# Kernel optimization log

Measured on AMD Instinct MI355X. Metric: run time of the kernel, lower is better.

The kernel has to match this reference:

```python
import jax, jax.numpy as jnp
import numpy as np

D_MODEL = 1024
D_FF = 4 * D_MODEL
NUM_EXPERTS = 8
TOP_K = 2
B, L = 4, 2048


def setup_inputs() -> dict:
    key = jax.random.key(0)
    ks = jax.random.split(key, 7)
    s = 0.02
    return {
        "x": jax.random.normal(ks[0], (B, L, D_MODEL), dtype=jnp.float32),
        "Wr": jax.random.normal(ks[1], (D_MODEL, NUM_EXPERTS), dtype=jnp.float32) * s,
        "br": jnp.zeros((NUM_EXPERTS,), dtype=jnp.float32),
        "W1": jax.random.normal(ks[2], (NUM_EXPERTS, D_MODEL, D_FF), dtype=jnp.float32) * s,
        "b1": jnp.zeros((NUM_EXPERTS, D_FF), dtype=jnp.float32),
        "W2": jax.random.normal(ks[3], (NUM_EXPERTS, D_FF, D_MODEL), dtype=jnp.float32) * s,
        "b2": jnp.zeros((NUM_EXPERTS, D_MODEL), dtype=jnp.float32),
    }


def reference(x, Wr, br, W1, b1, W2, b2):
    Bb, Ll, D = x.shape
    x_flat = x.reshape(-1, D)                      # [T, D]
    T = x_flat.shape[0]

    # Router: softmax over experts, then top-k and renormalize (matches torch)
    logits = x_flat @ Wr + br                      # [T, E]
    probs = jax.nn.softmax(logits, axis=-1)
    topk_w, topk_idx = jax.lax.top_k(probs, TOP_K)  # [T, K]
    topk_w = topk_w / jnp.sum(topk_w, axis=-1, keepdims=True)

    # Per-token per-expert combine weights: w_full[t, e] = sum_k topk_w[t,k] * (topk_idx[t,k]==e)
    # (top_k indices are distinct, so scatter-add equals the masked-overwrite loop)
    w_full = jnp.zeros((T, NUM_EXPERTS), dtype=x.dtype)
    rows = jnp.arange(T)[:, None]
    w_full = w_full.at[rows, topk_idx].add(topk_w)

    # Dense all-expert MLP (same math as masked per-expert dispatch; dropout is eval/no-op)
    h = jax.nn.gelu(jnp.einsum("td,edf->etf", x_flat, W1) + b1[:, None, :], approximate=False)
    y = jnp.einsum("etf,efd->etd", h, W2) + b2[:, None, :]   # [E, T, D]
    out = jnp.einsum("te,etd->td", w_full, y)                # [T, D]
    return out.reshape(Bb, Ll, D)
```

## Files before the change

### kernel.cpp

```cpp
#include <hip/hip_runtime.h>
#include <hip/hip_bf16.h>

#define T_TOKENS 8192
#define DM 1024
#define DF 4096
#define NE 8
#define NROWS 16384

typedef __attribute__((ext_vector_type(8))) short bf16x8;
typedef __attribute__((ext_vector_type(4))) float f32x4;

__device__ inline unsigned short f2bf(float f) {
  unsigned int u = __builtin_bit_cast(unsigned int, f);
  u = (u + 0x7fffu + ((u >> 16) & 1u)) >> 16;
  return (unsigned short)u;
}

__device__ inline float bf2f(unsigned short s) {
  unsigned int u = ((unsigned int)s) << 16;
  return __builtin_bit_cast(float, u);
}

__device__ __forceinline__ void gload16(const unsigned short* g, unsigned short* l) {
  __builtin_amdgcn_global_load_lds(
      (const __attribute__((address_space(1))) unsigned int*)g,
      (__attribute__((address_space(3))) unsigned int*)l,
      16, 0, 0);
}

__global__ void router_kernel(const float* __restrict__ x,
                              const float* __restrict__ Wr,
                              const float* __restrict__ br,
                              int* __restrict__ ctrl,
                              int* __restrict__ tope,
                              float* __restrict__ topw,
                              unsigned short* __restrict__ xb) {
  const int wid = threadIdx.x >> 6;
  const int lane = threadIdx.x & 63;
  const int t = blockIdx.x * 4 + wid;
  const float* xr = x + (size_t)t * DM;
  unsigned short* xbr = xb + (size_t)t * DM;
  float a[NE];
#pragma unroll
  for (int e = 0; e < NE; ++e) a[e] = 0.f;
#pragma unroll
  for (int it = 0; it < 4; ++it) {
    const int d0 = it * 256 + lane * 4;
    const float4 xv = *(const float4*)(xr + d0);
    ushort4 o;
    o.x = f2bf(xv.x); o.y = f2bf(xv.y); o.z = f2bf(xv.z); o.w = f2bf(xv.w);
    *(ushort4*)(xbr + d0) = o;
    const float xs[4] = {xv.x, xv.y, xv.z, xv.w};
#pragma unroll
    for (int j = 0; j < 4; ++j) {
      const float4 wa = *(const float4*)(Wr + (size_t)(d0 + j) * NE);
      const float4 wb = *(const float4*)(Wr + (size_t)(d0 + j) * NE + 4);
      a[0] += xs[j] * wa.x; a[1] += xs[j] * wa.y;
      a[2] += xs[j] * wa.z; a[3] += xs[j] * wa.w;
      a[4] += xs[j] * wb.x; a[5] += xs[j] * wb.y;
      a[6] += xs[j] * wb.z; a[7] += xs[j] * wb.w;
    }
  }
#pragma unroll
  for (int off = 32; off > 0; off >>= 1) {
#pragma unroll
    for (int e = 0; e < NE; ++e) a[e] += __shfl_xor(a[e], off);
  }
  if (lane == 0) {
    float lg[NE];
    float m = -1e30f;
#pragma unroll
    for (int e = 0; e < NE; ++e) { lg[e] = a[e] + br[e]; m = fmaxf(m, lg[e]); }
    float p[NE];
#pragma unroll
    for (int e = 0; e < NE; ++e) p[e] = expf(lg[e] - m);
    int i0 = 0;
#pragma unroll
    for (int e = 1; e < NE; ++e) if (p[e] > p[i0]) i0 = e;
    int i1 = (i0 == 0) ? 1 : 0;
#pragma unroll
    for (int e = 0; e < NE; ++e) if (e != i0 && p[e] > p[i1]) i1 = e;
    const float s = p[i0] + p[i1];
    tope[2 * t] = i0;
    tope[2 * t + 1] = i1;
    topw[2 * t] = p[i0] / s;
    topw[2 * t + 1] = p[i1] / s;
    atomicAdd(&ctrl[i0], 1);
    atomicAdd(&ctrl[i1], 1);
  }
}

__global__ void scan_kernel(int* __restrict__ ctrl) {
  if (threadIdx.x == 0 && blockIdx.x == 0) {
    int off = 0;
    for (int e = 0; e < NE; ++e) {
      ctrl[8 + e] = off;
      ctrl[20 + e] = off;
      off += ctrl[e];
    }
    ctrl[16] = off;
  }
}

__global__ void place_kernel(const int* __restrict__ tope,
                             const float* __restrict__ topw,
                             int* __restrict__ ctrl,
                             int* __restrict__ rowlist,
                             float* __restrict__ roww,
                             int* __restrict__ posmap) {
  const int t = blockIdx.x * blockDim.x + threadIdx.x;
#pragma unroll
  for (int k = 0; k < 2; ++k) {
    const int e = tope[2 * t + k];
    const int pos = atomicAdd(&ctrl[20 + e], 1);
    rowlist[pos] = t;
    roww[pos] = topw[2 * t + k];
    posmap[2 * t + k] = pos;
  }
}

__global__ void transpose_cvt_kernel(const float* __restrict__ in,
                                     unsigned short* __restrict__ outp,
                                     int R, int C) {
  __shared__ float tile[64][65];
  const int e = blockIdx.z;
  const int r0 = blockIdx.y * 64;
  const int c0 = blockIdx.x * 64;
  const float* src = in + ((size_t)e * R + r0) * C + c0;
#pragma unroll
  for (int i = 0; i < 16; ++i) {
    const int rr = (threadIdx.x >> 6) + i * 4;
    const int cc = threadIdx.x & 63;
    tile[rr][cc] = src[(size_t)rr * C + cc];
  }
  __syncthreads();
  unsigned short* dst = outp + ((size_t)e * C + c0) * R + r0;
#pragma unroll
  for (int i = 0; i < 8; ++i) {
    const int rr = (threadIdx.x >> 5) + i * 8;
    const int cc = (threadIdx.x & 31) * 2;
    const unsigned int lo = f2bf(tile[cc][rr]);
    const unsigned int hi = f2bf(tile[cc + 1][rr]);
    *(unsigned int*)(dst + (size_t)rr * R + cc) = lo | (hi << 16);
  }
}

__global__ __launch_bounds__(256, 2) void gemm1_kernel(
    const unsigned short* __restrict__ xb,
    const unsigned short* __restrict__ w1t,
    const float* __restrict__ b1,
    const int* __restrict__ ctrl,
    const int* __restrict__ rowlist,
    unsigned short* __restrict__ h) {
  const int e = blockIdx.z;
  const int count = ctrl[e];
  const int mt = blockIdx.y;
  if (mt * 128 >= count) return;
  const int off = ctrl[8 + e];
  const int n0 = blockIdx.x * 128;
  const int tid = threadIdx.x;
  const int wid = tid >> 6;
  const int lane = tid & 63;
  const int wm = (wid & 1) * 64;
  const int wn = (wid >> 1) * 64;
  const int q = lane >> 4;
  const int l16 = lane & 15;
  const int rl = lane >> 3;
  const int ch = lane & 7;

  __shared__ __attribute__((aligned(16))) unsigned short lA[128 * 64];
  __shared__ __attribute__((aligned(16))) unsigned short lB[128 * 64];

  const unsigned short* aBase[4];
  const unsigned short* bBase[4];
  unsigned short* lABase[4];
  unsigned short* lBBase[4];
#pragma unroll
  for (int i = 0; i < 4; ++i) {
    const int r = wid * 32 + i * 8 + rl;
    int rr = mt * 128 + r;
    if (rr >= count) rr = count - 1;
    const int tok = rowlist[off + rr];
    aBase[i] = xb + (size_t)tok * DM + ch * 8;
    bBase[i] = w1t + ((size_t)e * DF + n0 + r) * DM + ch * 8;
    lABase[i] = &lA[(wid * 32 + i * 8) * 64];
    lBBase[i] = &lB[(wid * 32 + i * 8) * 64];
  }

  f32x4 acc[4][4];
  const f32x4 z = {0.f, 0.f, 0.f, 0.f};
#pragma unroll
  for (int im = 0; im < 4; ++im)
#pragma unroll
    for (int in = 0; in < 4; ++in) acc[im][in] = z;

  for (int k0 = 0; k0 < DM; k0 += 64) {
#pragma unroll
    for (int i = 0; i < 4; ++i) gload16(aBase[i] + k0, lABase[i]);
#pragma unroll
    for (int i = 0; i < 4; ++i) gload16(bBase[i] + k0, lBBase[i]);
    __syncthreads();
#pragma unroll
    for (int ks = 0; ks < 2; ++ks) {
      bf16x8 af[4], bfr[4];
#pragma unroll
      for (int im = 0; im < 4; ++im)
        af[im] = *(const bf16x8*)&lA[(wm + im * 16 + l16) * 64 + ks * 32 + q * 8];
#pragma unroll
      for (int in = 0; in < 4; ++in)
        bfr[in] = *(const bf16x8*)&lB[(wn + in * 16 + l16) * 64 + ks * 32 + q * 8];
#pragma unroll
      for (int im = 0; im < 4; ++im)
#pragma unroll
        for (int in = 0; in < 4; ++in)
          acc[im][in] = __builtin_amdgcn_mfma_f32_16x16x32_bf16(
              af[im], bfr[in], acc[im][in], 0, 0, 0);
    }
    __syncthreads();
  }

#pragma unroll
  for (int in = 0; in < 4; ++in) {
    const int col = n0 + wn + in * 16 + l16;
    const float bias = b1[(size_t)e * DF + col];
#pragma unroll
    for (int im = 0; im < 4; ++im) {
      const int rbase = mt * 128 + wm + im * 16 + q * 4;
#pragma unroll
      for (int r2 = 0; r2 < 4; ++r2) {
        const int r = rbase + r2;
        if (r < count) {
          const float v = acc[im][in][r2] + bias;
          const float g = 0.5f * v * (1.0f + erff(v * 0.70710678118f));
          h[((size_t)(off + r)) * DF + col] = f2bf(g);
        }
      }
    }
  }
}

__global__ __launch_bounds__(256, 2) void gemm2_kernel(
    const unsigned short* __restrict__ h,
    const unsigned short* __restrict__ w2t,
    const float* __restrict__ b2,
    const int* __restrict__ ctrl,
    unsigned short* __restrict__ y) {
  const int e = blockIdx.z;
  const int count = ctrl[e];
  const int mt = blockIdx.y;
  if (mt * 128 >= count) return;
  const int off = ctrl[8 + e];
  const int n0 = blockIdx.x * 128;
  const int tid = threadIdx.x;
  const int wid = tid >> 6;
  const int lane = tid & 63;
  const int wm = (wid & 1) * 64;
  const int wn = (wid >> 1) * 64;
  const int q = lane >> 4;
  const int l16 = lane & 15;
  const int rl = lane >> 3;
  const int ch = lane & 7;

  __shared__ __attribute__((aligned(16))) unsigned short lA[128 * 64];
  __shared__ __attribute__((aligned(16))) unsigned short lB[128 * 64];

  const unsigned short* aBase[4];
  const unsigned short* bBase[4];
  unsigned short* lABase[4];
  unsigned short* lBBase[4];
#pragma unroll
  for (int i = 0; i < 4; ++i) {
    const int r = wid * 32 + i * 8 + rl;
    int rr = mt * 128 + r;
    if (rr >= count) rr = count - 1;
    aBase[i] = h + (size_t)(off + rr) * DF + ch * 8;
    bBase[i] = w2t + ((size_t)e * DM + n0 + r) * DF + ch * 8;
    lABase[i] = &lA[(wid * 32 + i * 8) * 64];
    lBBase[i] = &lB[(wid * 32 + i * 8) * 64];
  }

  f32x4 acc[4][4];
  const f32x4 z = {0.f, 0.f, 0.f, 0.f};
#pragma unroll
  for (int im = 0; im < 4; ++im)
#pragma unroll
    for (int in = 0; in < 4; ++in) acc[im][in] = z;

  for (int k0 = 0; k0 < DF; k0 += 64) {
#pragma unroll
    for (int i = 0; i < 4; ++i) gload16(aBase[i] + k0, lABase[i]);
#pragma unroll
    for (int i = 0; i < 4; ++i) gload16(bBase[i] + k0, lBBase[i]);
    __syncthreads();
#pragma unroll
    for (int ks = 0; ks < 2; ++ks) {
      bf16x8 af[4], bfr[4];
#pragma unroll
      for (int im = 0; im < 4; ++im)
        af[im] = *(const bf16x8*)&lA[(wm + im * 16 + l16) * 64 + ks * 32 + q * 8];
#pragma unroll
      for (int in = 0; in < 4; ++in)
        bfr[in] = *(const bf16x8*)&lB[(wn + in * 16 + l16) * 64 + ks * 32 + q * 8];
#pragma unroll
      for (int im = 0; im < 4; ++im)
#pragma unroll
        for (int in = 0; in < 4; ++in)
          acc[im][in] = __builtin_amdgcn_mfma_f32_16x16x32_bf16(
              af[im], bfr[in], acc[im][in], 0, 0, 0);
    }
    __syncthreads();
  }

#pragma unroll
  for (int in = 0; in < 4; ++in) {
    const int col = n0 + wn + in * 16 + l16;
    const float bias = b2[(size_t)e * DM + col];
#pragma unroll
    for (int im = 0; im < 4; ++im) {
      const int rbase = mt * 128 + wm + im * 16 + q * 4;
#pragma unroll
      for (int r2 = 0; r2 < 4; ++r2) {
        const int r = rbase + r2;
        if (r < count) {
          y[(size_t)(off + r) * DM + col] = f2bf(acc[im][in][r2] + bias);
        }
      }
    }
  }
}

__global__ void combine_kernel(const unsigned short* __restrict__ y,
                               const int* __restrict__ posmap,
                               const float* __restrict__ topw,
                               float* __restrict__ out) {
  const int t = blockIdx.x;
  const int c = threadIdx.x * 4;
  const int p0 = posmap[2 * t];
  const int p1 = posmap[2 * t + 1];
  const float w0 = topw[2 * t];
  const float w1 = topw[2 * t + 1];
  const ushort4 a = *(const ushort4*)(y + (size_t)p0 * DM + c);
  const ushort4 b = *(const ushort4*)(y + (size_t)p1 * DM + c);
  float4 o;
  o.x = w0 * bf2f(a.x) + w1 * bf2f(b.x);
  o.y = w0 * bf2f(a.y) + w1 * bf2f(b.y);
  o.z = w0 * bf2f(a.z) + w1 * bf2f(b.z);
  o.w = w0 * bf2f(a.w) + w1 * bf2f(b.w);
  *(float4*)(out + (size_t)t * DM + c) = o;
}

extern "C" void kernel_launch(void* const* d_in, const int* in_sizes, int n_in,
                              void* d_out, int out_size, void* d_ws, size_t ws_size,
                              hipStream_t stream) {
  const float* x  = (const float*)d_in[0];
  const float* Wr = (const float*)d_in[1];
  const float* br = (const float*)d_in[2];
  const float* W1 = (const float*)d_in[3];
  const float* b1 = (const float*)d_in[4];
  const float* W2 = (const float*)d_in[5];
  const float* b2 = (const float*)d_in[6];
  float* out = (float*)d_out;

  char* p = (char*)d_ws;
  auto alloc = [&](size_t bytes) -> char* {
    char* r = p;
    p += (bytes + 255) & ~(size_t)255;
    return r;
  };
  int* ctrl = (int*)alloc(1024);
  int* tope = (int*)alloc((size_t)2 * T_TOKENS * 4);
  float* topw = (float*)alloc((size_t)2 * T_TOKENS * 4);
  int* rowlist = (int*)alloc((size_t)NROWS * 4);
  float* roww = (float*)alloc((size_t)NROWS * 4);
  int* posmap = (int*)alloc((size_t)NROWS * 4);
  unsigned short* xb  = (unsigned short*)alloc((size_t)T_TOKENS * DM * 2);
  unsigned short* w1t = (unsigned short*)alloc((size_t)NE * DF * DM * 2);
  unsigned short* w2t = (unsigned short*)alloc((size_t)NE * DM * DF * 2);
  unsigned short* h   = (unsigned short*)alloc((size_t)NROWS * DF * 2);
  if ((size_t)(p - (char*)d_ws) > ws_size) return;

  unsigned short* y = w1t;

  hipMemsetAsync(ctrl, 0, 1024, stream);

  router_kernel<<<T_TOKENS / 4, 256, 0, stream>>>(x, Wr, br, ctrl, tope, topw, xb);
  scan_kernel<<<1, 64, 0, stream>>>(ctrl);
  place_kernel<<<T_TOKENS / 256, 256, 0, stream>>>(tope, topw, ctrl, rowlist, roww, posmap);
  transpose_cvt_kernel<<<dim3(DF / 64, DM / 64, NE), 256, 0, stream>>>(W1, w1t, DM, DF);
  transpose_cvt_kernel<<<dim3(DM / 64, DF / 64, NE), 256, 0, stream>>>(W2, w2t, DF, DM);
  gemm1_kernel<<<dim3(DF / 128, 64, NE), 256, 0, stream>>>(xb, w1t, b1, ctrl, rowlist, h);
  gemm2_kernel<<<dim3(DM / 128, 64, NE), 256, 0, stream>>>(h, w2t, b2, ctrl, y);
  combine_kernel<<<T_TOKENS, 256, 0, stream>>>(y, posmap, topw, out);
}
```

Before: 1.122 ms.

## Swizzle LDS tiles, transpose MFMA operands for vector stores, raise occupancy

Applies an XOR swizzle to the 16-byte chunk column in both the global-to-LDS loads and the fragment reads, to cut LDS bank conflicts when MFMA fragments are read. Swaps the MFMA A/B operands so each lane holds four consecutive output columns, which lets the epilogue write packed ushort4 stores and load bias as float4 instead of scattered 2-byte stores. It also raises the launch-bounds occupancy hint from 2 to 4 blocks per CU, which may force register spilling given the 64-float accumulator per thread.

After: 1.213 ms. +8.1%, slower.

```diff
diff --git a/kernel.cpp b/kernel.cpp
--- a/kernel.cpp
+++ b/kernel.cpp
@@ -145,7 +145,7 @@
   }
 }
 
-__global__ __launch_bounds__(256, 2) void gemm1_kernel(
+__global__ __launch_bounds__(256, 4) void gemm1_kernel(
     const unsigned short* __restrict__ xb,
     const unsigned short* __restrict__ w1t,
     const float* __restrict__ b1,
@@ -167,6 +167,7 @@
   const int l16 = lane & 15;
   const int rl = lane >> 3;
   const int ch = lane & 7;
+  const int sch = ch ^ rl;
 
   __shared__ __attribute__((aligned(16))) unsigned short lA[128 * 64];
   __shared__ __attribute__((aligned(16))) unsigned short lB[128 * 64];
@@ -181,8 +182,8 @@
     int rr = mt * 128 + r;
     if (rr >= count) rr = count - 1;
     const int tok = rowlist[off + rr];
-    aBase[i] = xb + (size_t)tok * DM + ch * 8;
-    bBase[i] = w1t + ((size_t)e * DF + n0 + r) * DM + ch * 8;
+    aBase[i] = xb + (size_t)tok * DM + sch * 8;
+    bBase[i] = w1t + ((size_t)e * DF + n0 + r) * DM + sch * 8;
     lABase[i] = &lA[(wid * 32 + i * 8) * 64];
     lBBase[i] = &lB[(wid * 32 + i * 8) * 64];
   }
@@ -202,44 +203,48 @@
     __syncthreads();
 #pragma unroll
     for (int ks = 0; ks < 2; ++ks) {
+      const int pc = ((ks * 4 + q) ^ (l16 & 7)) * 8;
       bf16x8 af[4], bfr[4];
 #pragma unroll
       for (int im = 0; im < 4; ++im)
-        af[im] = *(const bf16x8*)&lA[(wm + im * 16 + l16) * 64 + ks * 32 + q * 8];
+        af[im] = *(const bf16x8*)&lA[(wm + im * 16 + l16) * 64 + pc];
 #pragma unroll
       for (int in = 0; in < 4; ++in)
-        bfr[in] = *(const bf16x8*)&lB[(wn + in * 16 + l16) * 64 + ks * 32 + q * 8];
+        bfr[in] = *(const bf16x8*)&lB[(wn + in * 16 + l16) * 64 + pc];
 #pragma unroll
       for (int im = 0; im < 4; ++im)
 #pragma unroll
         for (int in = 0; in < 4; ++in)
           acc[im][in] = __builtin_amdgcn_mfma_f32_16x16x32_bf16(
-              af[im], bfr[in], acc[im][in], 0, 0, 0);
+              bfr[in], af[im], acc[im][in], 0, 0, 0);
     }
     __syncthreads();
   }
 
 #pragma unroll
-  for (int in = 0; in < 4; ++in) {
-    const int col = n0 + wn + in * 16 + l16;
-    const float bias = b1[(size_t)e * DF + col];
-#pragma unroll
-    for (int im = 0; im < 4; ++im) {
-      const int rbase = mt * 128 + wm + im * 16 + q * 4;
-#pragma unroll
-      for (int r2 = 0; r2 < 4; ++r2) {
-        const int r = rbase + r2;
-        if (r < count) {
-          const float v = acc[im][in][r2] + bias;
-          const float g = 0.5f * v * (1.0f + erff(v * 0.70710678118f));
-          h[((size_t)(off + r)) * DF + col] = f2bf(g);
-        }
+  for (int im = 0; im < 4; ++im) {
+    const int r = mt * 128 + wm + im * 16 + l16;
+    if (r < count) {
+      unsigned short* hrow = h + ((size_t)(off + r)) * DF + n0 + wn + q * 4;
+#pragma unroll
+      for (int in = 0; in < 4; ++in) {
+        const float4 bv = *(const float4*)(b1 + (size_t)e * DF + n0 + wn + in * 16 + q * 4);
+        float v0 = acc[im][in][0] + bv.x;
+        float v1 = acc[im][in][1] + bv.y;
+        float v2 = acc[im][in][2] + bv.z;
+        float v3 = acc[im][in][3] + bv.w;
+        ushort4 o;
+        o.x = f2bf(0.5f * v0 * (1.0f + erff(v0 * 0.70710678118f)));
+        o.y = f2bf(0.5f * v1 * (1.0f + erff(v1 * 0.70710678118f)));
+        o.z = f2bf(0.5f * v2 * (1.0f + erff(v2 * 0.70710678118f)));
+        o.w = f2bf(0.5f * v3 * (1.0f + erff(v3 * 0.70710678118f)));
+        *(ushort4*)(hrow + in * 16) = o;
       }
     }
   }
 }
 
-__global__ __launch_bounds__(256, 2) void gemm2_kernel(
+__global__ __launch_bounds__(256, 4) void gemm2_kernel(
     const unsigned short* __restrict__ h,
     const unsigned short* __restrict__ w2t,
     const float* __restrict__ b2,
@@ -260,6 +265,7 @@
   const int l16 = lane & 15;
   const int rl = lane >> 3;
   const int ch = lane & 7;
+  const int sch = ch ^ rl;
 
   __shared__ __attribute__((aligned(16))) unsigned short lA[128 * 64];
   __shared__ __attribute__((aligned(16))) unsigned short lB[128 * 64];
@@ -273,8 +279,8 @@
     const int r = wid * 32 + i * 8 + rl;
     int rr = mt * 128 + r;
     if (rr >= count) rr = count - 1;
-    aBase[i] = h + (size_t)(off + rr) * DF + ch * 8;
-    bBase[i] = w2t + ((size_t)e * DM + n0 + r) * DF + ch * 8;
+    aBase[i] = h + (size_t)(off + rr) * DF + sch * 8;
+    bBase[i] = w2t + ((size_t)e * DM + n0 + r) * DF + sch * 8;
     lABase[i] = &lA[(wid * 32 + i * 8) * 64];
     lBBase[i] = &lB[(wid * 32 + i * 8) * 64];
   }
@@ -294,36 +300,38 @@
     __syncthreads();
 #pragma unroll
     for (int ks = 0; ks < 2; ++ks) {
+      const int pc = ((ks * 4 + q) ^ (l16 & 7)) * 8;
       bf16x8 af[4], bfr[4];
 #pragma unroll
       for (int im = 0; im < 4; ++im)
-        af[im] = *(const bf16x8*)&lA[(wm + im * 16 + l16) * 64 + ks * 32 + q * 8];
+        af[im] = *(const bf16x8*)&lA[(wm + im * 16 + l16) * 64 + pc];
 #pragma unroll
       for (int in = 0; in < 4; ++in)
-        bfr[in] = *(const bf16x8*)&lB[(wn + in * 16 + l16) * 64 + ks * 32 + q * 8];
+        bfr[in] = *(const bf16x8*)&lB[(wn + in * 16 + l16) * 64 + pc];
 #pragma unroll
       for (int im = 0; im < 4; ++im)
 #pragma unroll
         for (int in = 0; in < 4; ++in)
           acc[im][in] = __builtin_amdgcn_mfma_f32_16x16x32_bf16(
-              af[im], bfr[in], acc[im][in], 0, 0, 0);
+              bfr[in], af[im], acc[im][in], 0, 0, 0);
     }
     __syncthreads();
   }
 
 #pragma unroll
-  for (int in = 0; in < 4; ++in) {
-    const int col = n0 + wn + in * 16 + l16;
-    const float bias = b2[(size_t)e * DM + col];
-#pragma unroll
-    for (int im = 0; im < 4; ++im) {
-      const int rbase = mt * 128 + wm + im * 16 + q * 4;
-#pragma unroll
-      for (int r2 = 0; r2 < 4; ++r2) {
-        const int r = rbase + r2;
-        if (r < count) {
-          y[(size_t)(off + r) * DM + col] = f2bf(acc[im][in][r2] + bias);
-        }
+  for (int im = 0; im < 4; ++im) {
+    const int r = mt * 128 + wm + im * 16 + l16;
+    if (r < count) {
+      unsigned short* yrow = y + ((size_t)(off + r)) * DM + n0 + wn + q * 4;
+#pragma unroll
+      for (int in = 0; in < 4; ++in) {
+        const float4 bv = *(const float4*)(b2 + (size_t)e * DM + n0 + wn + in * 16 + q * 4);
+        ushort4 o;
+        o.x = f2bf(acc[im][in][0] + bv.x);
+        o.y = f2bf(acc[im][in][1] + bv.y);
+        o.z = f2bf(acc[im][in][2] + bv.z);
+        o.w = f2bf(acc[im][in][3] + bv.w);
+        *(ushort4*)(yrow + in * 16) = o;
       }
     }
   }
```
